# Optimization experiments

Hardware: AMD Instinct MI355X
Metric: run time of the kernel (lower is better)

Reference implementation:

```python
import jax, jax.numpy as jnp
import numpy as np

NUM_NODES = 512
NUM_EDGES = 512
EMB_DIM = 128
HIDDEN = 256
NUM_INC = 8192


def setup_inputs() -> dict:
    key = jax.random.key(0)
    ks = jax.random.split(key, 8)
    X = jax.random.normal(ks[0], (NUM_NODES, EMB_DIM), dtype=jnp.float32)
    V = jax.random.randint(ks[1], (NUM_INC,), 0, NUM_NODES, dtype=jnp.int64)
    E = jax.random.randint(ks[2], (NUM_INC,), 0, NUM_EDGES, dtype=jnp.int64)
    # MLP params, torch nn.Linear layout: W (out, in), y = x @ W.T + b
    lim1 = 1.0 / np.sqrt(2 * EMB_DIM)
    W1 = jax.random.uniform(ks[3], (HIDDEN, 2 * EMB_DIM), minval=-lim1, maxval=lim1, dtype=jnp.float32)
    b1 = jax.random.uniform(ks[4], (HIDDEN,), minval=-lim1, maxval=lim1, dtype=jnp.float32)
    lim2 = 1.0 / np.sqrt(HIDDEN)
    W2 = jax.random.uniform(ks[5], (1, HIDDEN), minval=-lim2, maxval=lim2, dtype=jnp.float32)
    b2 = jax.random.uniform(ks[6], (1,), minval=-lim2, maxval=lim2, dtype=jnp.float32)
    return {"X": X, "V": V, "E": E, "W1": W1, "b1": b1, "W2": W2, "b2": b2}


def reference(X, V, E, W1, b1, W2, b2):
    d = X.shape[-1]
    # scatter-mean of gathered node embeddings into edges; empty edges -> 0 (nan_to_num)
    sums = jax.ops.segment_sum(X[V], E, num_segments=NUM_EDGES)          # (M, d)
    cnt = jax.ops.segment_sum(jnp.ones((V.shape[0],), X.dtype), E, num_segments=NUM_EDGES)
    eX = jnp.where(cnt[:, None] > 0, sums / jnp.maximum(cnt[:, None], 1.0), 0.0)
    # cat([X_expanded, eX_expanded]) @ W1.T == X @ W1[:, :d].T + eX @ W1[:, d:].T (broadcast add)
    hX = X @ W1[:, :d].T                                                 # (N, H)
    hE = eX @ W1[:, d:].T                                                # (M, H)
    hidden = jax.nn.relu(hX[:, None, :] + hE[None, :, :] + b1)           # (N, M, H)
    logits = jnp.einsum('nmh,h->nm', hidden, W2[0]) + b2[0]              # (N, M)
    prob = jax.nn.sigmoid(logits)
    prob = jnp.nan_to_num(prob, nan=0.5)
    prob = jnp.clip(prob, 1e-6, 1.0 - 1e-6)
    return prob
```

## Files before the change

kernel.cpp:

```cpp
#include <hip/hip_runtime.h>
#include <math.h>

#define NN 512
#define MM 512
#define DD 128
#define HH 256

#define WS_SUMS 0
#define WS_CNT  (MM * DD)
#define WS_A    (WS_CNT + MM)
#define WS_C    (WS_A + NN * HH)

__global__ __launch_bounds__(256) void k_scatter(
    const float* __restrict__ X, const int* __restrict__ V,
    const int* __restrict__ E, float* __restrict__ sums,
    float* __restrict__ cnt)
{
    int tid = blockIdx.x * 256 + threadIdx.x;
    int i = tid >> 7;
    int d = tid & 127;
    int v = V[i];
    int e = E[i];
    atomicAdd(&sums[e * DD + d], X[v * DD + d]);
    if (d == 0) atomicAdd(&cnt[e], 1.0f);
}

__global__ __launch_bounds__(256) void k_rows(
    const float* __restrict__ X, const float* __restrict__ W1,
    const float* __restrict__ b1, const float* __restrict__ sums,
    const float* __restrict__ cnt, float* __restrict__ A,
    float* __restrict__ C)
{
    int b = blockIdx.x;
    int h = threadIdx.x;
    int r0 = (b & 127) * 4;
    float acc0 = 0.f, acc1 = 0.f, acc2 = 0.f, acc3 = 0.f;

    if (b < 128) {
        const float* w  = W1 + h * (2 * DD);
        const float* x0 = X + (r0 + 0) * DD;
        const float* x1 = X + (r0 + 1) * DD;
        const float* x2 = X + (r0 + 2) * DD;
        const float* x3 = X + (r0 + 3) * DD;
        #pragma unroll 4
        for (int k = 0; k < DD; k += 4) {
            float4 wv = *(const float4*)(w + k);
            float4 v0 = *(const float4*)(x0 + k);
            float4 v1 = *(const float4*)(x1 + k);
            float4 v2 = *(const float4*)(x2 + k);
            float4 v3 = *(const float4*)(x3 + k);
            acc0 += wv.x * v0.x + wv.y * v0.y + wv.z * v0.z + wv.w * v0.w;
            acc1 += wv.x * v1.x + wv.y * v1.y + wv.z * v1.z + wv.w * v1.w;
            acc2 += wv.x * v2.x + wv.y * v2.y + wv.z * v2.z + wv.w * v2.w;
            acc3 += wv.x * v3.x + wv.y * v3.y + wv.z * v3.z + wv.w * v3.w;
        }
        A[(r0 + 0) * HH + h] = acc0;
        A[(r0 + 1) * HH + h] = acc1;
        A[(r0 + 2) * HH + h] = acc2;
        A[(r0 + 3) * HH + h] = acc3;
    } else {
        const float* w  = W1 + h * (2 * DD) + DD;
        float c0 = cnt[r0 + 0], c1 = cnt[r0 + 1], c2 = cnt[r0 + 2], c3 = cnt[r0 + 3];
        float i0 = c0 > 0.5f ? 1.0f / c0 : 0.0f;
        float i1 = c1 > 0.5f ? 1.0f / c1 : 0.0f;
        float i2 = c2 > 0.5f ? 1.0f / c2 : 0.0f;
        float i3 = c3 > 0.5f ? 1.0f / c3 : 0.0f;
        const float* s0 = sums + (r0 + 0) * DD;
        const float* s1 = sums + (r0 + 1) * DD;
        const float* s2 = sums + (r0 + 2) * DD;
        const float* s3 = sums + (r0 + 3) * DD;
        #pragma unroll 4
        for (int k = 0; k < DD; k += 4) {
            float4 wv = *(const float4*)(w + k);
            float4 v0 = *(const float4*)(s0 + k);
            float4 v1 = *(const float4*)(s1 + k);
            float4 v2 = *(const float4*)(s2 + k);
            float4 v3 = *(const float4*)(s3 + k);
            acc0 += wv.x * v0.x + wv.y * v0.y + wv.z * v0.z + wv.w * v0.w;
            acc1 += wv.x * v1.x + wv.y * v1.y + wv.z * v1.z + wv.w * v1.w;
            acc2 += wv.x * v2.x + wv.y * v2.y + wv.z * v2.z + wv.w * v2.w;
            acc3 += wv.x * v3.x + wv.y * v3.y + wv.z * v3.z + wv.w * v3.w;
        }
        float bb = b1[h];
        C[(r0 + 0) * HH + h] = acc0 * i0 + bb;
        C[(r0 + 1) * HH + h] = acc1 * i1 + bb;
        C[(r0 + 2) * HH + h] = acc2 * i2 + bb;
        C[(r0 + 3) * HH + h] = acc3 * i3 + bb;
    }
}

__global__ __launch_bounds__(256) void k_pairs(
    const float* __restrict__ A, const float* __restrict__ C,
    const float* __restrict__ W2, const float* __restrict__ b2,
    float* __restrict__ out)
{
    __shared__ float lds[16384];
    const int tid = threadIdx.x;
    const int bx = blockIdx.x;
    const int tn0 = (bx >> 4) * 32;
    const int tm0 = (bx & 15) * 32;

    #pragma unroll 4
    for (int r = 0; r < 32; ++r) {
        int sh = tid ^ (r & 28);
        lds[r * 256 + sh]        = A[(tn0 + r) * HH + tid];
        lds[8192 + r * 256 + sh] = C[(tm0 + r) * HH + tid];
    }
    __syncthreads();

    const int w    = tid >> 6;
    const int lane = tid & 63;
    const int tr   = lane & 7;
    const int tc   = lane >> 3;
    const int ra   = 4 * tr;
    const int rc   = 4 * tc;
    const int h0   = w * 64;

    float acc[4][4];
    #pragma unroll
    for (int i = 0; i < 4; ++i)
        #pragma unroll
        for (int j = 0; j < 4; ++j) acc[i][j] = 0.f;

    const float* la = lds + ra * 256;
    const float* lc = lds + 8192 + rc * 256;

    #pragma unroll 2
    for (int hh = 0; hh < 64; hh += 4) {
        int h = h0 + hh;
        float4 wv = *(const float4*)(W2 + h);
        int sa = h ^ ra;
        int sc = h ^ rc;
        float4 av[4], cv[4];
        #pragma unroll
        for (int i = 0; i < 4; ++i) av[i] = *(const float4*)(la + i * 256 + sa);
        #pragma unroll
        for (int j = 0; j < 4; ++j) cv[j] = *(const float4*)(lc + j * 256 + sc);
        #pragma unroll
        for (int i = 0; i < 4; ++i)
            #pragma unroll
            for (int j = 0; j < 4; ++j) {
                acc[i][j] += wv.x * fmaxf(av[i].x + cv[j].x, 0.f);
                acc[i][j] += wv.y * fmaxf(av[i].y + cv[j].y, 0.f);
                acc[i][j] += wv.z * fmaxf(av[i].z + cv[j].z, 0.f);
                acc[i][j] += wv.w * fmaxf(av[i].w + cv[j].w, 0.f);
            }
    }

    __syncthreads();
    #pragma unroll
    for (int i = 0; i < 4; ++i)
        #pragma unroll
        for (int j = 0; j < 4; ++j)
            lds[(i * 4 + j) * 256 + w * 64 + lane] = acc[i][j];
    __syncthreads();

    const float b2v = b2[0];
    const int lane0 = tid & 63;
    const int wq = tid >> 6;
    float4 s;
    float* sp = &s.x;
    #pragma unroll
    for (int kk = 0; kk < 4; ++kk) {
        int k = wq * 4 + kk;
        float t = 0.f;
        #pragma unroll
        for (int ww = 0; ww < 4; ++ww) t += lds[k * 256 + ww * 64 + lane0];
        float logit = t + b2v;
        float p = 1.0f / (1.0f + __expf(-logit));
        p = fminf(fmaxf(p, 1e-6f), 1.0f - 1e-6f);
        sp[kk] = p;
    }
    int r = 4 * (lane0 & 7) + wq;
    int c = 4 * (lane0 >> 3);
    *(float4*)(out + (tn0 + r) * MM + tm0 + c) = s;
}

extern "C" void kernel_launch(void* const* d_in, const int* in_sizes, int n_in,
                              void* d_out, int out_size, void* d_ws, size_t ws_size,
                              hipStream_t stream)
{
    const float* X  = (const float*)d_in[0];
    const int*   V  = (const int*)d_in[1];
    const int*   E  = (const int*)d_in[2];
    const float* W1 = (const float*)d_in[3];
    const float* b1 = (const float*)d_in[4];
    const float* W2 = (const float*)d_in[5];
    const float* b2 = (const float*)d_in[6];

    float* ws   = (float*)d_ws;
    float* sums = ws + WS_SUMS;
    float* cnt  = ws + WS_CNT;
    float* A    = ws + WS_A;
    float* C    = ws + WS_C;
    float* out  = (float*)d_out;

    hipMemsetAsync(d_ws, 0, (MM * DD + MM) * sizeof(float), stream);

    int ninc = in_sizes[1];
    k_scatter<<<(ninc * DD) / 256, 256, 0, stream>>>(X, V, E, sums, cnt);
    k_rows<<<256, 256, 0, stream>>>(X, W1, b1, sums, cnt, A, C);
    k_pairs<<<256, 256, 0, stream>>>(A, C, W2, b2, out);
}
```

Measured before the change: 94.63 us.

## Replace atomic scatter with per-edge gather and fuse into row projection; shrink pair tiles

Drops the memset and the atomic scatter kernel. Each edge block now scans all incidences to build an LDS list of its members, gathers and averages the node rows, and projects the mean through W1 in the same kernel, which also computes the node-side projections. This removes a launch, the memset and global atomic contention, but every edge block rereads the full E array. The pair kernel moves from 32x32 to 16x16 output tiles (1024 blocks, smaller LDS, float4 staging) to raise occupancy and block count, at the cost of lower per-thread reuse.

```diff
diff --git a/kernel.cpp b/kernel.cpp
--- a/kernel.cpp
+++ b/kernel.cpp
@@ -6,42 +6,65 @@
 #define DD 128
 #define HH 256
 
-#define WS_SUMS 0
-#define WS_CNT  (MM * DD)
-#define WS_A    (WS_CNT + MM)
-#define WS_C    (WS_A + NN * HH)
+#define WS_A 0
+#define WS_C (NN * HH)
 
-__global__ __launch_bounds__(256) void k_scatter(
+__global__ __launch_bounds__(256) void k_stage(
     const float* __restrict__ X, const int* __restrict__ V,
-    const int* __restrict__ E, float* __restrict__ sums,
-    float* __restrict__ cnt)
+    const int* __restrict__ E, const float* __restrict__ W1,
+    const float* __restrict__ b1, float* __restrict__ A,
+    float* __restrict__ C, int ninc)
 {
-    int tid = blockIdx.x * 256 + threadIdx.x;
-    int i = tid >> 7;
-    int d = tid & 127;
-    int v = V[i];
-    int e = E[i];
-    atomicAdd(&sums[e * DD + d], X[v * DD + d]);
-    if (d == 0) atomicAdd(&cnt[e], 1.0f);
-}
+    __shared__ int   lst[8192];
+    __shared__ float eXp[2 * DD];
+    __shared__ float eXs[DD];
+    __shared__ int   cnt_s;
 
-__global__ __launch_bounds__(256) void k_rows(
-    const float* __restrict__ X, const float* __restrict__ W1,
-    const float* __restrict__ b1, const float* __restrict__ sums,
-    const float* __restrict__ cnt, float* __restrict__ A,
-    float* __restrict__ C)
-{
-    int b = blockIdx.x;
-    int h = threadIdx.x;
-    int r0 = (b & 127) * 4;
-    float acc0 = 0.f, acc1 = 0.f, acc2 = 0.f, acc3 = 0.f;
+    const int b = blockIdx.x;
+    const int t = threadIdx.x;
 
-    if (b < 128) {
-        const float* w  = W1 + h * (2 * DD);
+    if (b < MM) {
+        if (t == 0) cnt_s = 0;
+        __syncthreads();
+        for (int i = t; i < ninc; i += 256)
+            if (E[i] == b) lst[atomicAdd(&cnt_s, 1)] = i;
+        __syncthreads();
+        const int cnt = cnt_s;
+
+        const int d = t & 127, half = t >> 7;
+        float a0 = 0.f, a1 = 0.f;
+        int j = half;
+        for (; j + 2 < cnt; j += 4) {
+            int i0 = lst[j], i1 = lst[j + 2];
+            a0 += X[V[i0] * DD + d];
+            a1 += X[V[i1] * DD + d];
+        }
+        for (; j < cnt; j += 2) a0 += X[V[lst[j]] * DD + d];
+        eXp[half * DD + d] = a0 + a1;
+        __syncthreads();
+        if (t < DD) {
+            float inv = cnt > 0 ? 1.0f / (float)cnt : 0.0f;
+            eXs[t] = (eXp[t] + eXp[DD + t]) * inv;
+        }
+        __syncthreads();
+
+        const float* w = W1 + t * (2 * DD) + DD;
+        float dot = b1[t];
+        #pragma unroll 8
+        for (int k = 0; k < DD; k += 4) {
+            float4 wv = *(const float4*)(w + k);
+            float4 ev = *(const float4*)(&eXs[k]);
+            dot += wv.x * ev.x + wv.y * ev.y + wv.z * ev.z + wv.w * ev.w;
+        }
+        C[b * HH + t] = dot;
+    } else {
+        const int r0 = (b - MM) * 4;
+        const float* w  = W1 + t * (2 * DD);
         const float* x0 = X + (r0 + 0) * DD;
         const float* x1 = X + (r0 + 1) * DD;
         const float* x2 = X + (r0 + 2) * DD;
         const float* x3 = X + (r0 + 3) * DD;
+        float acc0 = 0.f, acc1 = 0.f, acc2 = 0.f, acc3 = 0.f;
         #pragma unroll 4
         for (int k = 0; k < DD; k += 4) {
             float4 wv = *(const float4*)(w + k);
@@ -54,38 +77,10 @@
             acc2 += wv.x * v2.x + wv.y * v2.y + wv.z * v2.z + wv.w * v2.w;
             acc3 += wv.x * v3.x + wv.y * v3.y + wv.z * v3.z + wv.w * v3.w;
         }
-        A[(r0 + 0) * HH + h] = acc0;
-        A[(r0 + 1) * HH + h] = acc1;
-        A[(r0 + 2) * HH + h] = acc2;
-        A[(r0 + 3) * HH + h] = acc3;
-    } else {
-        const float* w  = W1 + h * (2 * DD) + DD;
-        float c0 = cnt[r0 + 0], c1 = cnt[r0 + 1], c2 = cnt[r0 + 2], c3 = cnt[r0 + 3];
-        float i0 = c0 > 0.5f ? 1.0f / c0 : 0.0f;
-        float i1 = c1 > 0.5f ? 1.0f / c1 : 0.0f;
-        float i2 = c2 > 0.5f ? 1.0f / c2 : 0.0f;
-        float i3 = c3 > 0.5f ? 1.0f / c3 : 0.0f;
-        const float* s0 = sums + (r0 + 0) * DD;
-        const float* s1 = sums + (r0 + 1) * DD;
-        const float* s2 = sums + (r0 + 2) * DD;
-        const float* s3 = sums + (r0 + 3) * DD;
-        #pragma unroll 4
-        for (int k = 0; k < DD; k += 4) {
-            float4 wv = *(const float4*)(w + k);
-            float4 v0 = *(const float4*)(s0 + k);
-            float4 v1 = *(const float4*)(s1 + k);
-            float4 v2 = *(const float4*)(s2 + k);
-            float4 v3 = *(const float4*)(s3 + k);
-            acc0 += wv.x * v0.x + wv.y * v0.y + wv.z * v0.z + wv.w * v0.w;
-            acc1 += wv.x * v1.x + wv.y * v1.y + wv.z * v1.z + wv.w * v1.w;
-            acc2 += wv.x * v2.x + wv.y * v2.y + wv.z * v2.z + wv.w * v2.w;
-            acc3 += wv.x * v3.x + wv.y * v3.y + wv.z * v3.z + wv.w * v3.w;
-        }
-        float bb = b1[h];
-        C[(r0 + 0) * HH + h] = acc0 * i0 + bb;
-        C[(r0 + 1) * HH + h] = acc1 * i1 + bb;
-        C[(r0 + 2) * HH + h] = acc2 * i2 + bb;
-        C[(r0 + 3) * HH + h] = acc3 * i3 + bb;
+        A[(r0 + 0) * HH + t] = acc0;
+        A[(r0 + 1) * HH + t] = acc1;
+        A[(r0 + 2) * HH + t] = acc2;
+        A[(r0 + 3) * HH + t] = acc3;
     }
 }
 
@@ -94,86 +89,65 @@
     const float* __restrict__ W2, const float* __restrict__ b2,
     float* __restrict__ out)
 {
-    __shared__ float lds[16384];
+    __shared__ float lds[8192];
     const int tid = threadIdx.x;
-    const int bx = blockIdx.x;
-    const int tn0 = (bx >> 4) * 32;
-    const int tm0 = (bx & 15) * 32;
+    const int bx  = blockIdx.x;
+    const int tn0 = (bx >> 5) * 16;
+    const int tm0 = (bx & 31) * 16;
 
-    #pragma unroll 4
-    for (int r = 0; r < 32; ++r) {
-        int sh = tid ^ (r & 28);
-        lds[r * 256 + sh]        = A[(tn0 + r) * HH + tid];
-        lds[8192 + r * 256 + sh] = C[(tm0 + r) * HH + tid];
+    {
+        const int c0 = (tid & 63) * 4;
+        const int rw = tid >> 6;
+        #pragma unroll
+        for (int p = 0; p < 4; ++p) {
+            int r  = p * 4 + rw;
+            int sh = c0 ^ (r & 28);
+            *(float4*)&lds[r * 256 + sh]        = *(const float4*)&A[(tn0 + r) * HH + c0];
+            *(float4*)&lds[4096 + r * 256 + sh] = *(const float4*)&C[(tm0 + r) * HH + c0];
+        }
     }
     __syncthreads();
 
-    const int w    = tid >> 6;
-    const int lane = tid & 63;
-    const int tr   = lane & 7;
-    const int tc   = lane >> 3;
-    const int ra   = 4 * tr;
-    const int rc   = 4 * tc;
-    const int h0   = w * 64;
+    const int w = tid >> 6, lane = tid & 63;
+    const int ra = 2 * (lane & 7);
+    const int rc = 2 * (lane >> 3);
+    const int pa = ra & 28, pc = rc & 28;
+    const int h0 = w * 64;
 
-    float acc[4][4];
-    #pragma unroll
-    for (int i = 0; i < 4; ++i)
-        #pragma unroll
-        for (int j = 0; j < 4; ++j) acc[i][j] = 0.f;
+    float a00 = 0.f, a01 = 0.f, a10 = 0.f, a11 = 0.f;
+    const float* la = lds + ra * 256;
+    const float* lc = lds + 4096 + rc * 256;
 
-    const float* la = lds + ra * 256;
-    const float* lc = lds + 8192 + rc * 256;
-
-    #pragma unroll 2
+    #pragma unroll 4
     for (int hh = 0; hh < 64; hh += 4) {
         int h = h0 + hh;
-        float4 wv = *(const float4*)(W2 + h);
-        int sa = h ^ ra;
-        int sc = h ^ rc;
-        float4 av[4], cv[4];
-        #pragma unroll
-        for (int i = 0; i < 4; ++i) av[i] = *(const float4*)(la + i * 256 + sa);
-        #pragma unroll
-        for (int j = 0; j < 4; ++j) cv[j] = *(const float4*)(lc + j * 256 + sc);
-        #pragma unroll
-        for (int i = 0; i < 4; ++i)
-            #pragma unroll
-            for (int j = 0; j < 4; ++j) {
-                acc[i][j] += wv.x * fmaxf(av[i].x + cv[j].x, 0.f);
-                acc[i][j] += wv.y * fmaxf(av[i].y + cv[j].y, 0.f);
-                acc[i][j] += wv.z * fmaxf(av[i].z + cv[j].z, 0.f);
-                acc[i][j] += wv.w * fmaxf(av[i].w + cv[j].w, 0.f);
-            }
+        float4 wv  = *(const float4*)(W2 + h);
+        float4 av0 = *(const float4*)(la + (h ^ pa));
+        float4 av1 = *(const float4*)(la + 256 + (h ^ pa));
+        float4 cv0 = *(const float4*)(lc + (h ^ pc));
+        float4 cv1 = *(const float4*)(lc + 256 + (h ^ pc));
+        a00 += wv.x * fmaxf(av0.x + cv0.x, 0.f) + wv.y * fmaxf(av0.y + cv0.y, 0.f)
+             + wv.z * fmaxf(av0.z + cv0.z, 0.f) + wv.w * fmaxf(av0.w + cv0.w, 0.f);
+        a01 += wv.x * fmaxf(av0.x + cv1.x, 0.f) + wv.y * fmaxf(av0.y + cv1.y, 0.f)
+             + wv.z * fmaxf(av0.z + cv1.z, 0.f) + wv.w * fmaxf(av0.w + cv1.w, 0.f);
+        a10 += wv.x * fmaxf(av1.x + cv0.x, 0.f) + wv.y * fmaxf(av1.y + cv0.y, 0.f)
+             + wv.z * fmaxf(av1.z + cv0.z, 0.f) + wv.w * fmaxf(av1.w + cv0.w, 0.f);
+        a11 += wv.x * fmaxf(av1.x + cv1.x, 0.f) + wv.y * fmaxf(av1.y + cv1.y, 0.f)
+             + wv.z * fmaxf(av1.z + cv1.z, 0.f) + wv.w * fmaxf(av1.w + cv1.w, 0.f);
     }
 
     __syncthreads();
-    #pragma unroll
-    for (int i = 0; i < 4; ++i)
-        #pragma unroll
-        for (int j = 0; j < 4; ++j)
-            lds[(i * 4 + j) * 256 + w * 64 + lane] = acc[i][j];
+    lds[w * 256 + (ra + 0) * 16 + (rc + 0)] = a00;
+    lds[w * 256 + (ra + 0) * 16 + (rc + 1)] = a01;
+    lds[w * 256 + (ra + 1) * 16 + (rc + 0)] = a10;
+    lds[w * 256 + (ra + 1) * 16 + (rc + 1)] = a11;
     __syncthreads();
 
-    const float b2v = b2[0];
-    const int lane0 = tid & 63;
-    const int wq = tid >> 6;
-    float4 s;
-    float* sp = &s.x;
-    #pragma unroll
-    for (int kk = 0; kk < 4; ++kk) {
-        int k = wq * 4 + kk;
-        float t = 0.f;
-        #pragma unroll
-        for (int ww = 0; ww < 4; ++ww) t += lds[k * 256 + ww * 64 + lane0];
-        float logit = t + b2v;
-        float p = 1.0f / (1.0f + __expf(-logit));
-        p = fminf(fmaxf(p, 1e-6f), 1.0f - 1e-6f);
-        sp[kk] = p;
-    }
-    int r = 4 * (lane0 & 7) + wq;
-    int c = 4 * (lane0 >> 3);
-    *(float4*)(out + (tn0 + r) * MM + tm0 + c) = s;
+    const int p = tid;
+    float s = lds[p] + lds[256 + p] + lds[512 + p] + lds[768 + p] + b2[0];
+    float prob = 1.0f / (1.0f + __expf(-s));
+    prob = fminf(fmaxf(prob, 1e-6f), 1.0f - 1e-6f);
+    out[(tn0 + (p >> 4)) * MM + tm0 + (p & 15)] = prob;
 }
 
 extern "C" void kernel_launch(void* const* d_in, const int* in_sizes, int n_in,
@@ -188,17 +162,13 @@
     const float* W2 = (const float*)d_in[5];
     const float* b2 = (const float*)d_in[6];
 
-    float* ws   = (float*)d_ws;
-    float* sums = ws + WS_SUMS;
-    float* cnt  = ws + WS_CNT;
-    float* A    = ws + WS_A;
-    float* C    = ws + WS_C;
-    float* out  = (float*)d_out;
-
-    hipMemsetAsync(d_ws, 0, (MM * DD + MM) * sizeof(float), stream);
+    float* ws  = (float*)d_ws;
+    float* A   = ws + WS_A;
+    float* C   = ws + WS_C;
+    float* out = (float*)d_out;
 
     int ninc = in_sizes[1];
-    k_scatter<<<(ninc * DD) / 256, 256, 0, stream>>>(X, V, E, sums, cnt);
-    k_rows<<<256, 256, 0, stream>>>(X, W1, b1, sums, cnt, A, C);
-    k_pairs<<<256, 256, 0, stream>>>(A, C, W2, b2, out);
+
+    k_stage<<<MM + NN / 4, 256, 0, stream>>>(X, V, E, W1, b1, A, C, ninc);
+    k_pairs<<<(NN / 16) * (MM / 16), 256, 0, stream>>>(A, C, W2, b2, out);
 }
```

Result: no change. 93.83 us (-0.8%).
